# Kernel tuning notes

Hardware: AMD Instinct MI355X
Metric: run time of the kernel (lower is better)

Reference implementation:

```python
import jax, jax.numpy as jnp
import numpy as np

MATCH_TIMES = 4  # init kwarg match_times
BS, Q, G = 16, 32768, 64  # uniform num_gt per image (original is ragged)


def box_xyxy_to_cxcywh(x):
    x0, y0, x1, y1 = x[..., 0], x[..., 1], x[..., 2], x[..., 3]
    return jnp.stack([(x0 + x1) * 0.5, (y0 + y1) * 0.5, x1 - x0, y1 - y0], axis=-1)


def _l1_cdist(a, b):
    # a: [bs,Q,4], b: [bs,G,4] -> [bs,Q,G]
    return jnp.abs(a[:, :, None, :] - b[:, None, :, :]).sum(-1)


def _topk_smallest_idx(c, k):
    # c: [bs,Q,G]; k smallest along Q -> indices [bs,k,G] (matches torch.topk(dim=0, largest=False))
    _, idx = jax.lax.top_k(-jnp.transpose(c, (0, 2, 1)), k)  # [bs,G,k]
    return jnp.transpose(idx, (0, 2, 1))


def setup_inputs() -> dict:
    key = jax.random.key(0)
    k1, k2, k3, k4 = jax.random.split(key, 4)
    return {
        "pred_boxes": jax.random.uniform(k1, (BS, Q, 4), dtype=jnp.float32),
        "anchors": jax.random.uniform(k2, (BS, Q, 4), dtype=jnp.float32),
        "gt_boxes": jax.random.uniform(k3, (BS * G, 4), dtype=jnp.float32),
        "gt_labels": jax.random.randint(k4, (BS * G,), 0, 80),
    }


def reference(pred_boxes, anchors, gt_boxes, gt_labels):
    bs, q, _ = pred_boxes.shape
    g = gt_boxes.shape[0] // bs
    k = MATCH_TIMES

    gt_c = box_xyxy_to_cxcywh(gt_boxes).reshape(bs, g, 4)
    cost_bbox = _l1_cdist(box_xyxy_to_cxcywh(pred_boxes), gt_c)      # [bs,Q,G]
    cost_anchors = _l1_cdist(box_xyxy_to_cxcywh(anchors), gt_c)      # [bs,Q,G]

    ip = _topk_smallest_idx(cost_bbox, k)     # [bs,k,G]
    ia = _topk_smallest_idx(cost_anchors, k)  # [bs,k,G]

    # Original interleaving per match round m: pred row m (G vals) then anchor row m (G vals)
    idx_i = jnp.stack([ip, ia], axis=2).reshape(bs, k * 2 * g).astype(jnp.int32)  # [bs, 2kG]
    idx_j = jnp.broadcast_to(jnp.tile(jnp.arange(g, dtype=jnp.int32), 2 * k), (bs, 2 * k * g))
    return idx_i, idx_j
```

## Files before the change

### kernel.cpp

```cpp
#include <hip/hip_runtime.h>

typedef unsigned long long ull;

#define QN 32768
#define GN 64
#define BSN 16
#define KM 4
#define INF __builtin_inff()

#define GPB 8
#define NL  (GPB * 2)
#define NT  512
#define NW  (NT / 64)
#define QS  4
#define QC  (QN / QS)
#define QPT (QC / NT)
#define SUB 4
#define NB  (BSN * 8 * QS)
#define BUFCAP 128
#define WS_NEED ((size_t)NB * NL * KM * sizeof(ull))

__device__ __forceinline__ float bcast(float x) {
    return __uint_as_float(__builtin_amdgcn_readfirstlane(__float_as_uint(x)));
}

__device__ __forceinline__ void merge4f(float* a, const float* b) {
    float m0 = fminf(a[0], b[3]);
    float m1 = fminf(a[1], b[2]);
    float m2 = fminf(a[2], b[1]);
    float m3 = fminf(a[3], b[0]);
    float x0 = fminf(m0, m2), x2 = fmaxf(m0, m2);
    float x1 = fminf(m1, m3), x3 = fmaxf(m1, m3);
    a[0] = fminf(x0, x1); a[1] = fmaxf(x0, x1);
    a[2] = fminf(x2, x3); a[3] = fmaxf(x2, x3);
}

__device__ __forceinline__ void insf(float* r, float v) {
    if (v < r[3]) {
        r[3] = v; float t;
        if (r[3] < r[2]) { t = r[2]; r[2] = r[3]; r[3] = t; }
        if (r[2] < r[1]) { t = r[1]; r[1] = r[2]; r[2] = t; }
        if (r[1] < r[0]) { t = r[0]; r[0] = r[1]; r[1] = t; }
    }
}

__device__ __forceinline__ void ins_u64(ull* r, ull kk) {
    if (kk < r[3]) {
        r[3] = kk; ull t;
        if (r[3] < r[2]) { t = r[2]; r[2] = r[3]; r[3] = t; }
        if (r[2] < r[1]) { t = r[1]; r[1] = r[2]; r[2] = t; }
        if (r[1] < r[0]) { t = r[0]; r[0] = r[1]; r[1] = t; }
    }
}

__device__ __forceinline__ void eval16(
    const float* gx, const float* gy, const float* gw, const float* gh,
    float4 p, float4 a, float* c)
{
    float pcx = (p.x + p.z) * 0.5f, pcy = (p.y + p.w) * 0.5f;
    float pw  = p.z - p.x,          ph  = p.w - p.y;
    float acx = (a.x + a.z) * 0.5f, acy = (a.y + a.w) * 0.5f;
    float aw  = a.z - a.x,          ah  = a.w - a.y;
#pragma unroll
    for (int j = 0; j < GPB; ++j) {
        c[2*j]   = ((fabsf(pcx - gx[j]) + fabsf(pcy - gy[j]))
                    + fabsf(pw - gw[j])) + fabsf(ph - gh[j]);
        c[2*j+1] = ((fabsf(acx - gx[j]) + fabsf(acy - gy[j]))
                    + fabsf(aw - gw[j])) + fabsf(ah - gh[j]);
    }
}

__global__ __launch_bounds__(NT, 4) void matcher_scan(
    const float4* __restrict__ pred, const float4* __restrict__ anc,
    const float4* __restrict__ gt, ull* __restrict__ ws)
{
    __shared__ float mnAll[NL][NT];
    __shared__ float Ts[NL];
    __shared__ int   cnt[NL];
    __shared__ ull   buf[NL][BUFCAP];

    int L   = ((blockIdx.x & 7) << 6) | (blockIdx.x >> 3);
    int b   = L >> 5;
    int gc  = (L >> 2) & 7;
    int qs  = L & 3;
    int tid = threadIdx.x;

    float gx[GPB], gy[GPB], gw[GPB], gh[GPB];
#pragma unroll
    for (int j = 0; j < GPB; ++j) {
        float4 gb = gt[b * GN + gc * GPB + j];
        gx[j] = bcast((gb.x + gb.z) * 0.5f);
        gy[j] = bcast((gb.y + gb.w) * 0.5f);
        gw[j] = bcast(gb.z - gb.x);
        gh[j] = bcast(gb.w - gb.y);
    }

    const float4* pq = pred + (size_t)b * QN + qs * QC;
    const float4* aq = anc  + (size_t)b * QN + qs * QC;

    float mn[NL];
#pragma unroll
    for (int l = 0; l < NL; ++l) mn[l] = INF;

#pragma unroll
    for (int it = 0; it < SUB; it += 2) {
        int o0 = it * NT + tid, o1 = o0 + NT;
        float4 p0 = pq[o0], a0 = aq[o0], p1 = pq[o1], a1 = aq[o1];
        float c[NL];
        eval16(gx, gy, gw, gh, p0, a0, c);
#pragma unroll
        for (int l = 0; l < NL; ++l) mn[l] = fminf(mn[l], c[l]);
        eval16(gx, gy, gw, gh, p1, a1, c);
#pragma unroll
        for (int l = 0; l < NL; ++l) mn[l] = fminf(mn[l], c[l]);
    }
#pragma unroll
    for (int l = 0; l < NL; ++l) mnAll[l][tid] = mn[l];
    if (tid < NL) cnt[tid] = 0;
    __syncthreads();

    {
        int wv = tid >> 6, lane = tid & 63;
#pragma unroll
        for (int li = 0; li < 2; ++li) {
            int l = wv * 2 + li;
            float r[KM] = { INF, INF, INF, INF };
#pragma unroll
            for (int i = 0; i < 8; ++i) insf(r, mnAll[l][lane + 64 * i]);
#pragma unroll
            for (int off = 1; off < 64; off <<= 1) {
                float bb[KM];
#pragma unroll
                for (int s = 0; s < KM; ++s) bb[s] = __shfl_xor(r[s], off, 64);
                merge4f(r, bb);
            }
            if (lane == 0) Ts[l] = r[3];
        }
    }
    __syncthreads();

    float T[NL];
#pragma unroll
    for (int l = 0; l < NL; ++l) T[l] = bcast(Ts[l]);

    for (int it = 0; it < QPT; it += 2) {
        int o0 = it * NT + tid, o1 = o0 + NT;
        float4 p0 = pq[o0], a0 = aq[o0], p1 = pq[o1], a1 = aq[o1];
#pragma unroll
        for (int u = 0; u < 2; ++u) {
            float4 p = u ? p1 : p0;
            float4 a = u ? a1 : a0;
            int qg = qs * QC + (u ? o1 : o0);
            float c[NL];
            eval16(gx, gy, gw, gh, p, a, c);
#pragma unroll
            for (int l = 0; l < NL; ++l) {
                if (__ballot(c[l] <= T[l])) {
                    if (c[l] <= T[l]) {
                        int s = atomicAdd(&cnt[l], 1);
                        if (s < BUFCAP)
                            buf[l][s] = (((ull)__float_as_uint(c[l])) << 15)
                                        | (ull)(unsigned)qg;
                    }
                }
            }
        }
    }
    __syncthreads();

    if (tid < NL) {
        int l = tid;
        int n = cnt[l]; if (n > BUFCAP) n = BUFCAP;
        ull r[KM] = { ~0ull, ~0ull, ~0ull, ~0ull };
        for (int i = 0; i < n; ++i) ins_u64(r, buf[l][i]);
        ull* w = ws + ((size_t)L * NL + l) * KM;
#pragma unroll
        for (int s = 0; s < KM; ++s) w[s] = r[s];
    }
}

__global__ __launch_bounds__(256) void matcher_merge(
    const ull* __restrict__ ws, int* __restrict__ out)
{
    int t = blockIdx.x * 256 + threadIdx.x;
    if (t >= BSN * 8 * NL) return;
    int b  = t >> 7;
    int gc = (t >> 4) & 7;
    int l  = t & 15;

    ull r[KM];
    {
        int L0 = (b << 5) | (gc << 2);
        const ull* w = ws + ((size_t)L0 * NL + l) * KM;
#pragma unroll
        for (int s = 0; s < KM; ++s) r[s] = w[s];
    }
#pragma unroll
    for (int qs = 1; qs < QS; ++qs) {
        int L = (b << 5) | (gc << 2) | qs;
        const ull* w = ws + ((size_t)L * NL + l) * KM;
#pragma unroll
        for (int s = 0; s < KM; ++s) ins_u64(r, w[s]);
    }

    int gl = l >> 1, type = l & 1;
    int g = gc * GPB + gl;
    int base = b * (2 * KM * GN);
    int* out_j = out + BSN * 2 * KM * GN;
#pragma unroll
    for (int m = 0; m < KM; ++m) {
        int qi = (int)(r[m] & 32767ull);
        int pos = base + m * (2 * GN) + type * GN + g;
        out[pos]   = qi;
        out_j[pos] = g;
    }
}

__global__ __launch_bounds__(1024) void matcher_single(
    const float4* __restrict__ pred, const float4* __restrict__ anc,
    const float4* __restrict__ gt, int* __restrict__ out)
{
    __shared__ float fws4[8][16][KM];
    __shared__ float fTs[8];
    __shared__ int   fcnt[8];
    __shared__ ull   fbuf[8][64];

    int bid = blockIdx.x;
    int xcd = bid & 7;
    int k   = bid >> 3;
    int b   = (xcd << 1) | (k & 1);
    int gc  = k >> 1;
    int tid = threadIdx.x;

    float gx[4], gy[4], gw[4], gh[4];
#pragma unroll
    for (int j = 0; j < 4; ++j) {
        float4 gb = gt[b * GN + gc * 4 + j];
        gx[j] = (gb.x + gb.z) * 0.5f; gy[j] = (gb.y + gb.w) * 0.5f;
        gw[j] = gb.z - gb.x;          gh[j] = gb.w - gb.y;
    }
    const float4* pb = pred + (size_t)b * QN;
    const float4* ab = anc  + (size_t)b * QN;

    float mn[8];
#pragma unroll
    for (int l = 0; l < 8; ++l) mn[l] = INF;

    for (int q0 = tid; q0 < QN; q0 += 1024) {
        float4 p = pb[q0], a = ab[q0];
        float pcx=(p.x+p.z)*0.5f, pcy=(p.y+p.w)*0.5f, pw=p.z-p.x, ph=p.w-p.y;
        float acx=(a.x+a.z)*0.5f, acy=(a.y+a.w)*0.5f, aw=a.z-a.x, ah=a.w-a.y;
#pragma unroll
        for (int j = 0; j < 4; ++j) {
            mn[2*j]   = fminf(mn[2*j],   ((fabsf(pcx-gx[j])+fabsf(pcy-gy[j]))+fabsf(pw-gw[j]))+fabsf(ph-gh[j]));
            mn[2*j+1] = fminf(mn[2*j+1], ((fabsf(acx-gx[j])+fabsf(acy-gy[j]))+fabsf(aw-gw[j]))+fabsf(ah-gh[j]));
        }
    }

    float m4[8][KM];
#pragma unroll
    for (int l = 0; l < 8; ++l) { m4[l][0]=mn[l]; m4[l][1]=INF; m4[l][2]=INF; m4[l][3]=INF; }
#pragma unroll
    for (int off = 1; off < 64; off <<= 1) {
#pragma unroll
        for (int l = 0; l < 8; ++l) {
            float bb[KM];
#pragma unroll
            for (int s = 0; s < KM; ++s) bb[s] = __shfl_xor(m4[l][s], off, 64);
            merge4f(m4[l], bb);
        }
    }
    int lane = tid & 63, wv = tid >> 6;
    if (lane == 0)
#pragma unroll
        for (int l = 0; l < 8; ++l)
#pragma unroll
            for (int s = 0; s < KM; ++s) fws4[l][wv][s] = m4[l][s];
    if (tid < 8) fcnt[tid] = 0;
    __syncthreads();
    if (tid < 8) {
        float r[KM];
#pragma unroll
        for (int s = 0; s < KM; ++s) r[s] = fws4[tid][0][s];
        for (int w = 1; w < 16; ++w) merge4f(r, fws4[tid][w]);
        fTs[tid] = r[3];
    }
    __syncthreads();
    float T[8];
#pragma unroll
    for (int l = 0; l < 8; ++l) T[l] = fTs[l];

    for (int q0 = tid; q0 < QN; q0 += 1024) {
        float4 p = pb[q0], a = ab[q0];
        float pcx=(p.x+p.z)*0.5f, pcy=(p.y+p.w)*0.5f, pw=p.z-p.x, ph=p.w-p.y;
        float acx=(a.x+a.z)*0.5f, acy=(a.y+a.w)*0.5f, aw=a.z-a.x, ah=a.w-a.y;
#pragma unroll
        for (int j = 0; j < 4; ++j) {
            float cb = ((fabsf(pcx-gx[j])+fabsf(pcy-gy[j]))+fabsf(pw-gw[j]))+fabsf(ph-gh[j]);
            if (cb <= T[2*j]) {
                int s = atomicAdd(&fcnt[2*j], 1);
                if (s < 64) fbuf[2*j][s] = (((ull)__float_as_uint(cb)) << 15) | (ull)(unsigned)q0;
            }
            float ca = ((fabsf(acx-gx[j])+fabsf(acy-gy[j]))+fabsf(aw-gw[j]))+fabsf(ah-gh[j]);
            if (ca <= T[2*j+1]) {
                int s = atomicAdd(&fcnt[2*j+1], 1);
                if (s < 64) fbuf[2*j+1][s] = (((ull)__float_as_uint(ca)) << 15) | (ull)(unsigned)q0;
            }
        }
    }
    __syncthreads();

    if (tid < 8) {
        int l = tid, n = fcnt[l]; if (n > 64) n = 64;
        ull r[KM] = { ~0ull, ~0ull, ~0ull, ~0ull };
        for (int i = 0; i < n; ++i) ins_u64(r, fbuf[l][i]);
        int gl = l >> 1, type = l & 1;
        int g = gc * 4 + gl;
        int base = b * (2 * KM * GN);
        int* out_j = out + BSN * 2 * KM * GN;
#pragma unroll
        for (int m = 0; m < KM; ++m) {
            int qi = (int)(r[m] & 32767ull);
            int pos = base + m * (2 * GN) + type * GN + g;
            out[pos]   = qi;
            out_j[pos] = g;
        }
    }
}

extern "C" void kernel_launch(void* const* d_in, const int* in_sizes, int n_in,
                              void* d_out, int out_size, void* d_ws, size_t ws_size,
                              hipStream_t stream) {
    const float4* pred = (const float4*)d_in[0];
    const float4* anc  = (const float4*)d_in[1];
    const float4* gt   = (const float4*)d_in[2];
    int* out = (int*)d_out;

    if (ws_size >= WS_NEED) {
        ull* ws = (ull*)d_ws;
        matcher_scan<<<NB, NT, 0, stream>>>(pred, anc, gt, ws);
        matcher_merge<<<8, 256, 0, stream>>>(ws, out);
    } else {
        matcher_single<<<256, 1024, 0, stream>>>(pred, anc, gt, out);
    }
}
```

Measured before the change: 40.66 us.

## Split query range eight ways with smaller blocks, fold halving into FMA, pair ballots

Doubles the number of query slices per (image, gt-chunk), uses 256-thread blocks and shrinks the threshold sampling prefix, producing twice as many smaller blocks. The center computation is rewritten to keep unscaled sums and apply the 0.5 factor through an fmaf, and the candidate-collection ballot now tests the pred and anchor costs for each gt in one ballot. This aims for better occupancy and shorter per-block scans with fewer ALU ops and fewer ballots. In exchange the sampled threshold is looser, so more candidates may land in the buffers, and the merge kernel has twice as many partial lists to combine. Floating-point rounding of costs changes slightly, which could alter tie ordering.

```diff
diff --git a/kernel.cpp b/kernel.cpp
--- a/kernel.cpp
+++ b/kernel.cpp
@@ -10,12 +10,12 @@
 
 #define GPB 8
 #define NL  (GPB * 2)
-#define NT  512
+#define NT  256
 #define NW  (NT / 64)
-#define QS  4
+#define QS  8
 #define QC  (QN / QS)
 #define QPT (QC / NT)
-#define SUB 4
+#define SUB 2
 #define NB  (BSN * 8 * QS)
 #define BUFCAP 128
 #define WS_NEED ((size_t)NB * NL * KM * sizeof(ull))
@@ -54,19 +54,19 @@
 }
 
 __device__ __forceinline__ void eval16(
-    const float* gx, const float* gy, const float* gw, const float* gh,
+    const float* Gx, const float* Gy, const float* gw, const float* gh,
     float4 p, float4 a, float* c)
 {
-    float pcx = (p.x + p.z) * 0.5f, pcy = (p.y + p.w) * 0.5f;
-    float pw  = p.z - p.x,          ph  = p.w - p.y;
-    float acx = (a.x + a.z) * 0.5f, acy = (a.y + a.w) * 0.5f;
-    float aw  = a.z - a.x,          ah  = a.w - a.y;
+    float pSx = p.x + p.z, pSy = p.y + p.w;
+    float pw  = p.z - p.x, ph  = p.w - p.y;
+    float aSx = a.x + a.z, aSy = a.y + a.w;
+    float aw  = a.z - a.x, ah  = a.w - a.y;
 #pragma unroll
     for (int j = 0; j < GPB; ++j) {
-        c[2*j]   = ((fabsf(pcx - gx[j]) + fabsf(pcy - gy[j]))
-                    + fabsf(pw - gw[j])) + fabsf(ph - gh[j]);
-        c[2*j+1] = ((fabsf(acx - gx[j]) + fabsf(acy - gy[j]))
-                    + fabsf(aw - gw[j])) + fabsf(ah - gh[j]);
+        c[2*j]   = fmaf(0.5f, fabsf(pSx - Gx[j]) + fabsf(pSy - Gy[j]),
+                        fabsf(pw - gw[j])) + fabsf(ph - gh[j]);
+        c[2*j+1] = fmaf(0.5f, fabsf(aSx - Gx[j]) + fabsf(aSy - Gy[j]),
+                        fabsf(aw - gw[j])) + fabsf(ah - gh[j]);
     }
 }
 
@@ -79,18 +79,18 @@
     __shared__ int   cnt[NL];
     __shared__ ull   buf[NL][BUFCAP];
 
-    int L   = ((blockIdx.x & 7) << 6) | (blockIdx.x >> 3);
-    int b   = L >> 5;
-    int gc  = (L >> 2) & 7;
-    int qs  = L & 3;
+    int L   = ((blockIdx.x & 7) << 7) | (blockIdx.x >> 3);
+    int b   = L >> 6;
+    int gc  = (L >> 3) & 7;
+    int qs  = L & 7;
     int tid = threadIdx.x;
 
-    float gx[GPB], gy[GPB], gw[GPB], gh[GPB];
+    float Gx[GPB], Gy[GPB], gw[GPB], gh[GPB];
 #pragma unroll
     for (int j = 0; j < GPB; ++j) {
         float4 gb = gt[b * GN + gc * GPB + j];
-        gx[j] = bcast((gb.x + gb.z) * 0.5f);
-        gy[j] = bcast((gb.y + gb.w) * 0.5f);
+        Gx[j] = bcast(gb.x + gb.z);
+        Gy[j] = bcast(gb.y + gb.w);
         gw[j] = bcast(gb.z - gb.x);
         gh[j] = bcast(gb.w - gb.y);
     }
@@ -102,15 +102,14 @@
 #pragma unroll
     for (int l = 0; l < NL; ++l) mn[l] = INF;
 
-#pragma unroll
-    for (int it = 0; it < SUB; it += 2) {
-        int o0 = it * NT + tid, o1 = o0 + NT;
-        float4 p0 = pq[o0], a0 = aq[o0], p1 = pq[o1], a1 = aq[o1];
+    {
+        float4 p0 = pq[tid],      a0 = aq[tid];
+        float4 p1 = pq[NT + tid], a1 = aq[NT + tid];
         float c[NL];
-        eval16(gx, gy, gw, gh, p0, a0, c);
+        eval16(Gx, Gy, gw, gh, p0, a0, c);
 #pragma unroll
         for (int l = 0; l < NL; ++l) mn[l] = fminf(mn[l], c[l]);
-        eval16(gx, gy, gw, gh, p1, a1, c);
+        eval16(Gx, Gy, gw, gh, p1, a1, c);
 #pragma unroll
         for (int l = 0; l < NL; ++l) mn[l] = fminf(mn[l], c[l]);
     }
@@ -122,11 +121,11 @@
     {
         int wv = tid >> 6, lane = tid & 63;
 #pragma unroll
-        for (int li = 0; li < 2; ++li) {
-            int l = wv * 2 + li;
+        for (int li = 0; li < 4; ++li) {
+            int l = wv * 4 + li;
             float r[KM] = { INF, INF, INF, INF };
 #pragma unroll
-            for (int i = 0; i < 8; ++i) insf(r, mnAll[l][lane + 64 * i]);
+            for (int i = 0; i < NW; ++i) insf(r, mnAll[l][lane + 64 * i]);
 #pragma unroll
             for (int off = 1; off < 64; off <<= 1) {
                 float bb[KM];
@@ -152,15 +151,23 @@
             float4 a = u ? a1 : a0;
             int qg = qs * QC + (u ? o1 : o0);
             float c[NL];
-            eval16(gx, gy, gw, gh, p, a, c);
-#pragma unroll
-            for (int l = 0; l < NL; ++l) {
-                if (__ballot(c[l] <= T[l])) {
-                    if (c[l] <= T[l]) {
-                        int s = atomicAdd(&cnt[l], 1);
+            eval16(Gx, Gy, gw, gh, p, a, c);
+#pragma unroll
+            for (int j = 0; j < GPB; ++j) {
+                bool h0 = c[2*j]   <= T[2*j];
+                bool h1 = c[2*j+1] <= T[2*j+1];
+                if (__ballot(h0 || h1)) {
+                    if (h0) {
+                        int s = atomicAdd(&cnt[2*j], 1);
                         if (s < BUFCAP)
-                            buf[l][s] = (((ull)__float_as_uint(c[l])) << 15)
-                                        | (ull)(unsigned)qg;
+                            buf[2*j][s] = (((ull)__float_as_uint(c[2*j])) << 15)
+                                          | (ull)(unsigned)qg;
+                    }
+                    if (h1) {
+                        int s = atomicAdd(&cnt[2*j+1], 1);
+                        if (s < BUFCAP)
+                            buf[2*j+1][s] = (((ull)__float_as_uint(c[2*j+1])) << 15)
+                                            | (ull)(unsigned)qg;
                     }
                 }
             }
@@ -190,14 +197,14 @@
 
     ull r[KM];
     {
-        int L0 = (b << 5) | (gc << 2);
+        int L0 = (b << 6) | (gc << 3);
         const ull* w = ws + ((size_t)L0 * NL + l) * KM;
 #pragma unroll
         for (int s = 0; s < KM; ++s) r[s] = w[s];
     }
 #pragma unroll
     for (int qs = 1; qs < QS; ++qs) {
-        int L = (b << 5) | (gc << 2) | qs;
+        int L = (b << 6) | (gc << 3) | qs;
         const ull* w = ws + ((size_t)L * NL + l) * KM;
 #pragma unroll
         for (int s = 0; s < KM; ++s) ins_u64(r, w[s]);
```

Measured after the change: 59.21 us. +45.6%, slower.
